# Kernel optimization log

Measured on AMD Instinct MI355X. Metric: run time of the kernel, lower is better.

Reference implementation:

```python
import jax, jax.numpy as jnp
import numpy as np

T, B, OBS, H, A = 1024, 512, 64, 128, 16


def setup_inputs() -> dict:
    key = jax.random.key(0)
    ks = jax.random.split(key, 20)
    s = lambda fan_in: 1.0 / np.sqrt(fan_in)
    return {
        "hidden": jnp.zeros((B, H), jnp.float32),
        "obs": jax.random.normal(ks[0], (T, B, OBS), jnp.float32),
        "dones": jax.random.bernoulli(ks[1], 0.05, (T, B)),
        # embedding Dense
        "W_emb": jax.random.normal(ks[2], (OBS, H), jnp.float32) * s(OBS),
        "b_emb": jnp.zeros((H,), jnp.float32),
        # GRUCell: input kernels (r|z|n) with bias, hidden kernels (r|z|n), only n-gate hidden bias
        "Wi": jax.random.normal(ks[3], (H, 3 * H), jnp.float32) * s(H),
        "bi": jnp.zeros((3 * H,), jnp.float32),
        "Wh": jax.random.normal(ks[4], (H, 3 * H), jnp.float32) * s(H),
        "bh_n": jnp.zeros((H,), jnp.float32),
        # actor head
        "Wa1": jax.random.normal(ks[5], (H, H), jnp.float32) * s(H),
        "ba1": jnp.zeros((H,), jnp.float32),
        "Wa2": jax.random.normal(ks[6], (H, A), jnp.float32) * (0.01 * s(H)),
        "ba2": jnp.zeros((A,), jnp.float32),
        # critic head
        "Wc1": jax.random.normal(ks[7], (H, H), jnp.float32) * s(H),
        "bc1": jnp.zeros((H,), jnp.float32),
        "Wc2": jax.random.normal(ks[8], (H, 1), jnp.float32) * s(H),
        "bc2": jnp.zeros((1,), jnp.float32),
    }


def reference(hidden, obs, dones, W_emb, b_emb, Wi, bi, Wh, bh_n,
              Wa1, ba1, Wa2, ba2, Wc1, bc1, Wc2, bc2):
    # embedding: Dense + relu, applied to all timesteps at once  [T,B,H]
    emb = jax.nn.relu(jnp.einsum("tbo,oh->tbh", obs, W_emb) + b_emb)
    # precompute input-side gate projections for all steps  [T,B,3H]
    xi = jnp.einsum("tbh,hg->tbg", emb, Wi) + bi

    def step(h, xs):
        xi_t, done_t = xs
        h = jnp.where(done_t[:, None], 0.0, h)  # reset carry on done
        hh = h @ Wh  # [B,3H]
        xr, xz, xn = jnp.split(xi_t, 3, axis=-1)
        hr, hz, hn = jnp.split(hh, 3, axis=-1)
        r = jax.nn.sigmoid(xr + hr)
        z = jax.nn.sigmoid(xz + hz)
        n = jnp.tanh(xn + r * (hn + bh_n))
        h_new = (1.0 - z) * n + z * h
        return h_new, h_new

    hidden, y = jax.lax.scan(step, hidden, (xi, dones))  # y: [T,B,H]

    # actor head -> categorical logits [T,B,A]
    a1 = jax.nn.relu(jnp.einsum("tbh,hk->tbk", y, Wa1) + ba1)
    logits = jnp.einsum("tbh,ha->tba", a1, Wa2) + ba2
    # critic head -> value [T,B]
    c1 = jax.nn.relu(jnp.einsum("tbh,hk->tbk", y, Wc1) + bc1)
    v = jnp.squeeze(jnp.einsum("tbh,hk->tbk", c1, Wc2) + bc2, axis=-1)
    return (hidden, logits, v)
```

## Files before the change

### kernel.cpp

```cpp
#include <hip/hip_runtime.h>

#define T_DIM 1024
#define B_DIM 512
#define OBS_DIM 64
#define H_DIM 128
#define G3 384
#define A_DIM 16
#define CT 256
#define NCHUNK 4

typedef __bf16 bf16;
typedef __attribute__((ext_vector_type(4))) __bf16 bf16x4;
typedef __attribute__((ext_vector_type(8))) __bf16 bf16x8;
typedef __attribute__((ext_vector_type(4))) float f32x4;

#define MFMA(a, b, c) __builtin_amdgcn_mfma_f32_16x16x32_bf16((a), (b), (c), 0, 0, 0)

__device__ __forceinline__ float sigm(float x) { return 1.0f / (1.0f + __expf(-x)); }
__device__ __forceinline__ float tanh_f(float x) { return 1.0f - 2.0f / (__expf(2.0f * x) + 1.0f); }

__global__ __launch_bounds__(256) void prep_k(
    const float* __restrict__ hidden, const int* __restrict__ dones,
    const float* __restrict__ W_emb, const float* __restrict__ Wi,
    const float* __restrict__ Wh, const float* __restrict__ Wa1,
    const float* __restrict__ Wa2, const float* __restrict__ Wc1,
    const float* __restrict__ Wc2,
    bf16* __restrict__ wembT, bf16* __restrict__ wiT, bf16* __restrict__ whT,
    bf16* __restrict__ wa1T, bf16* __restrict__ wa2T, bf16* __restrict__ wc1T,
    bf16* __restrict__ wc2T, float* __restrict__ h_state) {
  int i = blockIdx.x * 256 + threadIdx.x;
  if (i < 8192) { int n = i / OBS_DIM, k = i % OBS_DIM; wembT[i] = (bf16)W_emb[k * H_DIM + n]; return; }
  i -= 8192;
  if (i < 49152) { int g = i / H_DIM, k = i % H_DIM; wiT[i] = (bf16)Wi[k * G3 + g]; return; }
  i -= 49152;
  if (i < 49152) { int g = i / H_DIM, k = i % H_DIM; whT[i] = (bf16)Wh[k * G3 + g]; return; }
  i -= 49152;
  if (i < 16384) { int n = i / H_DIM, k = i % H_DIM; wa1T[i] = (bf16)Wa1[k * H_DIM + n]; return; }
  i -= 16384;
  if (i < 2048) { int a = i / H_DIM, k = i % H_DIM; wa2T[i] = (bf16)Wa2[k * A_DIM + a]; return; }
  i -= 2048;
  if (i < 16384) { int n = i / H_DIM, k = i % H_DIM; wc1T[i] = (bf16)Wc1[k * H_DIM + n]; return; }
  i -= 16384;
  if (i < 2048) { int r = i / H_DIM, k = i % H_DIM; wc2T[i] = (r == 0) ? (bf16)Wc2[k] : (bf16)0.0f; return; }
  i -= 2048;
  if (i < 65536) { int b = i / H_DIM; h_state[i] = dones[b] ? 0.0f : hidden[i]; return; }
}


__device__ __forceinline__ void phase1_body(
    char* smem, int tile_base, int ntiles, const float* __restrict__ obs,
    const float* __restrict__ b_emb, const float* __restrict__ bi,
    const bf16* __restrict__ wembT, const bf16* __restrict__ wiT,
    bf16* __restrict__ xi, int row_base) {
  bf16 (*obs_lds)[72]  = (bf16(*)[72])smem;
  bf16 (*emb_lds)[136] = (bf16(*)[136])(smem + 2304);
  bf16 (*strip)[392]   = (bf16(*)[392])(smem + 6656);
  int tid = threadIdx.x, wave = tid >> 6, lane = tid & 63;
  int nl = lane & 15, q = lane >> 4;

  bf16x8 we[2][2], wi_f[6][4];
  float bev[2], biv[6];
#pragma unroll
  for (int e = 0; e < 2; ++e) {
    int nt = wave * 2 + e;
#pragma unroll
    for (int kb = 0; kb < 2; ++kb)
      we[e][kb] = *(const bf16x8*)(wembT + (nt * 16 + nl) * OBS_DIM + kb * 32 + q * 8);
    bev[e] = b_emb[nt * 16 + nl];
  }
#pragma unroll
  for (int j = 0; j < 6; ++j) {
    int nt = wave * 6 + j;
#pragma unroll
    for (int kb = 0; kb < 4; ++kb)
      wi_f[j][kb] = *(const bf16x8*)(wiT + (nt * 16 + nl) * H_DIM + kb * 32 + q * 8);
    biv[j] = bi[nt * 16 + nl];
  }

  int srow = tid >> 4, scol = (tid & 15) * 4;
  for (int rt = 0; rt < ntiles; ++rt) {
    int r0 = (tile_base + rt) * 16;
    {
      const float* src = obs + ((long)row_base + r0 + srow) * OBS_DIM + scol;
      float4 vv = *(const float4*)src;
      bf16x4 b; b[0] = (bf16)vv.x; b[1] = (bf16)vv.y; b[2] = (bf16)vv.z; b[3] = (bf16)vv.w;
      *(bf16x4*)&obs_lds[srow][scol] = b;
    }
    __syncthreads();
    bf16x8 ao[2];
#pragma unroll
    for (int kb = 0; kb < 2; ++kb) ao[kb] = *(const bf16x8*)&obs_lds[nl][kb * 32 + q * 8];
#pragma unroll
    for (int e = 0; e < 2; ++e) {
      f32x4 c = {0.f, 0.f, 0.f, 0.f};
      c = MFMA(ao[0], we[e][0], c);
      c = MFMA(ao[1], we[e][1], c);
#pragma unroll
      for (int r = 0; r < 4; ++r) {
        float v = c[r] + bev[e];
        emb_lds[q * 4 + r][(wave * 2 + e) * 16 + nl] = (bf16)(v > 0.f ? v : 0.f);
      }
    }
    __syncthreads();
    bf16x8 ae[4];
#pragma unroll
    for (int kb = 0; kb < 4; ++kb) ae[kb] = *(const bf16x8*)&emb_lds[nl][kb * 32 + q * 8];
#pragma unroll
    for (int j = 0; j < 6; ++j) {
      int nt = wave * 6 + j;
      f32x4 c = {0.f, 0.f, 0.f, 0.f};
#pragma unroll
      for (int kb = 0; kb < 4; ++kb) c = MFMA(ae[kb], wi_f[j][kb], c);
      int gate = nt >> 3, dloc = (nt & 7) * 16 + nl;
      int pos = (gate < 2) ? (2 * dloc + gate) : (256 + dloc);
#pragma unroll
      for (int r = 0; r < 4; ++r) strip[q * 4 + r][pos] = (bf16)(c[r] + biv[j]);
    }
    __syncthreads();
    bf16* dst = xi + (long)r0 * G3;
#pragma unroll
    for (int it = 0; it < 3; ++it) {
      int e0 = (it * 256 + tid) * 8;
      int row = e0 / G3, col = e0 % G3;
      *(int4*)(dst + e0) = *(const int4*)&strip[row][col];
    }
    __syncthreads();
  }
}

__device__ __forceinline__ void scan_body(
    char* smem, int bid, const bf16* __restrict__ xi,
    const int* __restrict__ dones, const float* __restrict__ bh_n,
    const bf16* __restrict__ whT, float* __restrict__ h_state,
    bf16* __restrict__ y, float* __restrict__ hidden_out, int chunk) {
  bf16 (*hb)[2][136]       = (bf16(*)[2][136])smem;
  bf16 (*xibuf)[8][2][400] = (bf16(*)[8][2][400])(smem + 1088);
  int  (*dn)[2]            = (int(*)[2])(smem + 26688);

  __builtin_amdgcn_s_setprio(1);

  int tid = threadIdx.x;
  int wave = tid >> 6, lane = tid & 63;
  int nl = lane & 15, q = lane >> 4;
  int b0 = bid * 2;
  int ch = q & 1;
  int hsel = q >> 1;
  int dim = wave * 16 + (hsel << 6) + nl;
  int hrow = nl & 1;

  for (int i = tid; i <= CT; i += 256) {
    int t = chunk * CT + i;
    dn[i][0] = (t < T_DIM) ? dones[t * B_DIM + b0] : 0;
    dn[i][1] = (t < T_DIM) ? dones[t * B_DIM + b0 + 1] : 0;
  }
  int c0 = tid, c1 = 256 + tid, c2 = 512 + tid;
  int t0 = c0 / 96, p0 = c0 % 96, sc0 = p0 / 48, o0 = (p0 % 48) * 8;
  int t1 = c1 / 96, p1 = c1 % 96, sc1 = p1 / 48, o1 = (p1 % 48) * 8;
  int t2 = c2 / 96, p2 = c2 % 96, sc2 = p2 / 48, o2 = (p2 % 48) * 8;
  const long PSTR = (long)8 * B_DIM * G3;
  const bf16* pfs0 = xi + ((long)(8 + t0) * B_DIM + b0 + sc0) * G3 + o0;
  const bf16* pfs1 = xi + ((long)(8 + t1) * B_DIM + b0 + sc1) * G3 + o1;
  const bf16* pfs2 = xi + ((long)(8 + t2) * B_DIM + b0 + sc2) * G3 + o2;
  *(int4*)&xibuf[0][t0][sc0][o0] = *(const int4*)(xi + ((long)t0 * B_DIM + b0 + sc0) * G3 + o0);
  *(int4*)&xibuf[0][t1][sc1][o1] = *(const int4*)(xi + ((long)t1 * B_DIM + b0 + sc1) * G3 + o1);
  *(int4*)&xibuf[0][t2][sc2][o2] = *(const int4*)(xi + ((long)t2 * B_DIM + b0 + sc2) * G3 + o2);

  float hprev = h_state[(b0 + ch) * H_DIM + dim];
  hb[0][ch][dim] = (bf16)hprev;

  bf16x8 wf[6][4];
#pragma unroll
  for (int g = 0; g < 3; ++g)
#pragma unroll
    for (int hI = 0; hI < 2; ++hI)
#pragma unroll
      for (int kb = 0; kb < 4; ++kb)
        wf[g * 2 + hI][kb] =
            *(const bf16x8*)(whT + ((g * 8 + wave + 4 * hI) * 16 + nl) * H_DIM + kb * 32 + q * 8);
  float bhn = bh_n[dim];
  bf16* yp = y + (long)(b0 + ch) * H_DIM + dim;
  __syncthreads();

  int4 pfr0, pfr1, pfr2;

#define BAR()                                                                  \
  do {                                                                         \
    asm volatile("s_waitcnt lgkmcnt(0)" ::: "memory");                         \
    __builtin_amdgcn_sched_barrier(0);                                         \
    __builtin_amdgcn_s_barrier();                                              \
    __builtin_amdgcn_sched_barrier(0);                                         \
  } while (0)

#define MSTEP(HA, KB)                                                          \
  do {                                                                         \
    c0_ = MFMA(HA, wf[0][KB], c0_); c1_ = MFMA(HA, wf[1][KB], c1_);            \
    c2_ = MFMA(HA, wf[2][KB], c2_); c3_ = MFMA(HA, wf[3][KB], c3_);            \
    c4_ = MFMA(HA, wf[4][KB], c4_); c5_ = MFMA(HA, wf[5][KB], c5_);            \
  } while (0)

#define GSTEP(CUR, TS, TB, PF)                                                 \
  do {                                                                         \
    const int p_ = (TS) & 1;                                                   \
    bf16x8 ha0 = *(const bf16x8*)&hb[p_][hrow][0 * 32 + q * 8];                \
    bf16x8 ha1 = *(const bf16x8*)&hb[p_][hrow][1 * 32 + q * 8];                \
    bf16x8 ha2 = *(const bf16x8*)&hb[p_][hrow][2 * 32 + q * 8];                \
    bf16x8 ha3 = *(const bf16x8*)&hb[p_][hrow][3 * 32 + q * 8];                \
    const bf16* xrow_ = &xibuf[CUR][TS][ch][0];                                \
    unsigned urz_ = *(const unsigned*)(xrow_ + 2 * dim);                       \
    float xnv_ = (float)xrow_[256 + dim];                                      \
    int dnv_ = dn[(TB) + (TS) + 1][ch];                                        \
    if ((TS) == 0 && (PF)) {                                                   \
      pfr0 = *(const int4*)pfs0; pfs0 += PSTR;                                 \
      pfr1 = *(const int4*)pfs1; pfs1 += PSTR;                                 \
      pfr2 = *(const int4*)pfs2; pfs2 += PSTR;                                 \
    }                                                                          \
    f32x4 c0_ = {0.f, 0.f, 0.f, 0.f}, c1_ = {0.f, 0.f, 0.f, 0.f};             \
    f32x4 c2_ = {0.f, 0.f, 0.f, 0.f}, c3_ = {0.f, 0.f, 0.f, 0.f};             \
    f32x4 c4_ = {0.f, 0.f, 0.f, 0.f}, c5_ = {0.f, 0.f, 0.f, 0.f};             \
    MSTEP(ha0, 0); MSTEP(ha1, 1); MSTEP(ha2, 2); MSTEP(ha3, 3);                \
    if ((TS) == 7 && (PF)) {                                                   \
      *(int4*)&xibuf[(CUR) ^ 1][t0][sc0][o0] = pfr0;                           \
      *(int4*)&xibuf[(CUR) ^ 1][t1][sc1][o1] = pfr1;                           \
      *(int4*)&xibuf[(CUR) ^ 1][t2][sc2][o2] = pfr2;                           \
    }                                                                          \
    float hr_ = hsel ? (ch ? c1_[1] : c1_[0]) : (ch ? c0_[1] : c0_[0]);        \
    float hz_ = hsel ? (ch ? c3_[1] : c3_[0]) : (ch ? c2_[1] : c2_[0]);        \
    float hn_ = hsel ? (ch ? c5_[1] : c5_[0]) : (ch ? c4_[1] : c4_[0]);        \
    union { unsigned u; float f; } cvr_, cvz_;                                 \
    cvr_.u = urz_ << 16; cvz_.u = urz_ & 0xffff0000u;                          \
    float r_ = sigm(cvr_.f + hr_);                                             \
    float z_ = sigm(cvz_.f + hz_);                                             \
    float n_ = tanh_f(xnv_ + r_ * (hn_ + bhn));                                \
    float hnew_ = (1.0f - z_) * n_ + z_ * hprev;                               \
    float heff_ = dnv_ ? 0.0f : hnew_;                                         \
    *yp = (bf16)hnew_; yp += B_DIM * H_DIM;                                    \
    hb[p_ ^ 1][ch][dim] = (bf16)heff_;                                         \
    hprev = heff_;                                                             \
    BAR();                                                                     \
  } while (0)

  for (int tb = 0; tb < CT; tb += 16) {
    GSTEP(0, 0, tb, 1); GSTEP(0, 1, tb, 1); GSTEP(0, 2, tb, 1); GSTEP(0, 3, tb, 1);
    GSTEP(0, 4, tb, 1); GSTEP(0, 5, tb, 1); GSTEP(0, 6, tb, 1); GSTEP(0, 7, tb, 1);
    const int pfB = (tb + 16 < CT) ? 1 : 0;
    GSTEP(1, 0, tb + 8, pfB); GSTEP(1, 1, tb + 8, pfB); GSTEP(1, 2, tb + 8, pfB);
    GSTEP(1, 3, tb + 8, pfB); GSTEP(1, 4, tb + 8, pfB); GSTEP(1, 5, tb + 8, pfB);
    GSTEP(1, 6, tb + 8, pfB); GSTEP(1, 7, tb + 8, pfB);
  }
#undef GSTEP
#undef MSTEP
#undef BAR
  __builtin_amdgcn_s_setprio(0);

  h_state[(b0 + ch) * H_DIM + dim] = hprev;
  if (chunk == NCHUNK - 1) hidden_out[(b0 + ch) * H_DIM + dim] = hprev;
}

__device__ __forceinline__ void heads_body(
    char* smem, int tile_base, int ntiles, const bf16* __restrict__ y,
    const float* __restrict__ ba1, const float* __restrict__ ba2,
    const float* __restrict__ bc1, const float* __restrict__ bc2,
    const bf16* __restrict__ wa1T, const bf16* __restrict__ wa2T,
    const bf16* __restrict__ wc1T, const bf16* __restrict__ wc2T,
    float* __restrict__ logits, float* __restrict__ v, int t_base) {
  bf16  (*y_lds)[136] = (bf16(*)[136])smem;
  bf16  (*a1s)[136]   = (bf16(*)[136])(smem + 4352);
  bf16  (*c1s)[136]   = (bf16(*)[136])(smem + 8704);
  float (*s_o)[16]    = (float(*)[16])(smem + 13056);
  float (*s_v)        = (float*)(smem + 14080);
  int tid = threadIdx.x, wave = tid >> 6, lane = tid & 63;
  int nl = lane & 15, q = lane >> 4;

  bf16x8 wa1f[2][4], wc1f[2][4], wa2f[4], wc2f[4];
  float ba1v[2], bc1v[2];
#pragma unroll
  for (int e = 0; e < 2; ++e) {
    int nt = wave * 2 + e;
#pragma unroll
    for (int kb = 0; kb < 4; ++kb) {
      wa1f[e][kb] = *(const bf16x8*)(wa1T + (nt * 16 + nl) * H_DIM + kb * 32 + q * 8);
      wc1f[e][kb] = *(const bf16x8*)(wc1T + (nt * 16 + nl) * H_DIM + kb * 32 + q * 8);
    }
    ba1v[e] = ba1[nt * 16 + nl];
    bc1v[e] = bc1[nt * 16 + nl];
  }
#pragma unroll
  for (int kb = 0; kb < 4; ++kb) {
    wa2f[kb] = *(const bf16x8*)(wa2T + nl * H_DIM + kb * 32 + q * 8);
    wc2f[kb] = *(const bf16x8*)(wc2T + nl * H_DIM + kb * 32 + q * 8);
  }
  float ba2v = ba2[nl], bc2v = bc2[0];

  int srow = tid >> 4, scol = (tid & 15) * 8;
  for (int rt = 0; rt < ntiles; ++rt) {
    int r0 = (tile_base + rt) * 16;
    long gr0 = (long)t_base * B_DIM + r0;
    *(int4*)&y_lds[srow][scol] = *(const int4*)(y + (long)(r0 + srow) * H_DIM + scol);
    __syncthreads();
    bf16x8 ya[4];
#pragma unroll
    for (int kb = 0; kb < 4; ++kb) ya[kb] = *(const bf16x8*)&y_lds[nl][kb * 32 + q * 8];
#pragma unroll
    for (int e = 0; e < 2; ++e) {
      f32x4 ca = {0.f, 0.f, 0.f, 0.f}, cc = {0.f, 0.f, 0.f, 0.f};
#pragma unroll
      for (int kb = 0; kb < 4; ++kb) {
        ca = MFMA(ya[kb], wa1f[e][kb], ca);
        cc = MFMA(ya[kb], wc1f[e][kb], cc);
      }
      int colb = (wave * 2 + e) * 16 + nl;
#pragma unroll
      for (int r = 0; r < 4; ++r) {
        float va = ca[r] + ba1v[e];
        float vc = cc[r] + bc1v[e];
        a1s[q * 4 + r][colb] = (bf16)(va > 0.f ? va : 0.f);
        c1s[q * 4 + r][colb] = (bf16)(vc > 0.f ? vc : 0.f);
      }
    }
    __syncthreads();
    if (wave == 0) {
      bf16x8 a1f[4];
#pragma unroll
      for (int kb = 0; kb < 4; ++kb) a1f[kb] = *(const bf16x8*)&a1s[nl][kb * 32 + q * 8];
      f32x4 c = {0.f, 0.f, 0.f, 0.f};
#pragma unroll
      for (int kb = 0; kb < 4; ++kb) c = MFMA(a1f[kb], wa2f[kb], c);
#pragma unroll
      for (int r = 0; r < 4; ++r) s_o[q * 4 + r][nl] = c[r] + ba2v;
    } else if (wave == 1) {
      bf16x8 c1f[4];
#pragma unroll
      for (int kb = 0; kb < 4; ++kb) c1f[kb] = *(const bf16x8*)&c1s[nl][kb * 32 + q * 8];
      f32x4 c = {0.f, 0.f, 0.f, 0.f};
#pragma unroll
      for (int kb = 0; kb < 4; ++kb) c = MFMA(c1f[kb], wc2f[kb], c);
      if (nl == 0) {
#pragma unroll
        for (int r = 0; r < 4; ++r) s_v[q * 4 + r] = c[r] + bc2v;
      }
    }
    __syncthreads();
    if (tid < 64) {
      *(int4*)(logits + gr0 * A_DIM + tid * 4) = *(const int4*)&s_o[tid >> 2][(tid & 3) * 4];
    } else if (tid < 80) {
      v[gr0 + (tid - 64)] = s_v[tid - 64];
    }
    __syncthreads();
  }
}

__global__ __launch_bounds__(256, 2) void fused_k(
    const float* __restrict__ obs, const float* __restrict__ b_emb,
    const float* __restrict__ bi, const bf16* __restrict__ wembT,
    const bf16* __restrict__ wiT, bf16* __restrict__ xi0, bf16* __restrict__ xi1,
    const int* __restrict__ dones, const float* __restrict__ bh_n,
    const bf16* __restrict__ whT, float* __restrict__ h_state,
    bf16* __restrict__ y0, bf16* __restrict__ y1, float* __restrict__ hidden_out,
    const float* __restrict__ ba1, const float* __restrict__ ba2,
    const float* __restrict__ bc1, const float* __restrict__ bc2,
    const bf16* __restrict__ wa1T, const bf16* __restrict__ wa2T,
    const bf16* __restrict__ wc1T, const bf16* __restrict__ wc2T,
    float* __restrict__ logits, float* __restrict__ v, int cs) {
  __shared__ __align__(16) char smem[50176];
  int bid = blockIdx.x;
  if (cs == -1) {
    phase1_body(smem, bid * 16, 16, obs, b_emb, bi, wembT, wiT, xi0, 0);
    return;
  }
  if (cs == NCHUNK) {
    heads_body(smem, bid * 16, 16, ((NCHUNK - 1) & 1) ? y1 : y0, ba1, ba2, bc1,
               bc2, wa1T, wa2T, wc1T, wc2T, logits, v, (NCHUNK - 1) * CT);
    return;
  }
  if (bid < 256) {
    scan_body(smem, bid, (cs & 1) ? xi1 : xi0, dones, bh_n, whT, h_state,
              (cs & 1) ? y1 : y0, hidden_out, cs);
    return;
  }
  {
    int wb = bid - 256;
    int cp = cs + 1;
    if (cp < NCHUNK)
      phase1_body(smem, wb * 32, 32, obs, b_emb, bi, wembT, wiT,
                  (cp & 1) ? xi1 : xi0, cp * CT * B_DIM);
    int ch2 = cs - 1;
    if (ch2 >= 0)
      heads_body(smem, wb * 32, 32, (ch2 & 1) ? y1 : y0, ba1, ba2, bc1, bc2,
                 wa1T, wa2T, wc1T, wc2T, logits, v, ch2 * CT);
  }
}

extern "C" void kernel_launch(void* const* d_in, const int* in_sizes, int n_in,
                              void* d_out, int out_size, void* d_ws, size_t ws_size,
                              hipStream_t stream) {
  const float* hidden = (const float*)d_in[0];
  const float* obs    = (const float*)d_in[1];
  const int*   dones  = (const int*)d_in[2];
  const float* W_emb  = (const float*)d_in[3];
  const float* b_emb  = (const float*)d_in[4];
  const float* Wi     = (const float*)d_in[5];
  const float* bi     = (const float*)d_in[6];
  const float* Wh     = (const float*)d_in[7];
  const float* bh_n   = (const float*)d_in[8];
  const float* Wa1    = (const float*)d_in[9];
  const float* ba1    = (const float*)d_in[10];
  const float* Wa2    = (const float*)d_in[11];
  const float* ba2    = (const float*)d_in[12];
  const float* Wc1    = (const float*)d_in[13];
  const float* bc1    = (const float*)d_in[14];
  const float* Wc2    = (const float*)d_in[15];
  const float* bc2    = (const float*)d_in[16];

  float* out_hidden = (float*)d_out;
  float* out_logits = out_hidden + B_DIM * H_DIM;
  float* out_v      = out_logits + (long)T_DIM * B_DIM * A_DIM;

  char* ws = (char*)d_ws;
  bf16*  wembT   = (bf16*)(ws + 0);
  bf16*  wiT     = (bf16*)(ws + 16384);
  bf16*  whT     = (bf16*)(ws + 114688);
  bf16*  wa1T    = (bf16*)(ws + 212992);
  bf16*  wa2T    = (bf16*)(ws + 245760);
  bf16*  wc1T    = (bf16*)(ws + 249856);
  bf16*  wc2T    = (bf16*)(ws + 282624);
  float* h_state = (float*)(ws + 286720);
  bf16*  xi0     = (bf16*)(ws + 548864);
  bf16*  xi1     = (bf16*)(ws + 101212160);
  bf16*  y0      = (bf16*)(ws + 201875456);
  bf16*  y1      = (bf16*)(ws + 235429888);

  prep_k<<<816, 256, 0, stream>>>(hidden, dones, W_emb, Wi, Wh, Wa1, Wa2, Wc1, Wc2,
                                  wembT, wiT, whT, wa1T, wa2T, wc1T, wc2T, h_state);
  for (int cs = -1; cs <= NCHUNK; ++cs) {
    fused_k<<<512, 256, 0, stream>>>(obs, b_emb, bi, wembT, wiT, xi0, xi1,
                                     dones, bh_n, whT, h_state, y0, y1, out_hidden,
                                     ba1, ba2, bc1, bc2, wa1T, wa2T, wc1T, wc2T,
                                     out_logits, out_v, cs);
  }
  (void)in_sizes; (void)n_in; (void)out_size; (void)ws_size;
}
```

Baseline: 748.1 us.

## Process four batch rows per scan block and halve grid to one block per CU

Each scan block now handles 4 batch rows instead of 2, using all four lanes groups of the MFMA output and computing two hidden dims per lane. The grid shrinks to 256 blocks (128 scan + 128 producer/heads) with launch bounds of one block per CU and a smaller LDS footprint, and prefetch blocks become 4 timesteps. This halves the number of weight-register copies and uses the MFMA rows more fully, but doubles the serial elementwise work per lane per step and reduces overall parallelism for the non-scan phases.

New measurement: 977.1 us. 1.31x slower.

```diff
diff --git a/kernel.cpp b/kernel.cpp
--- a/kernel.cpp
+++ b/kernel.cpp
@@ -18,6 +18,11 @@
 
 __device__ __forceinline__ float sigm(float x) { return 1.0f / (1.0f + __expf(-x)); }
 __device__ __forceinline__ float tanh_f(float x) { return 1.0f - 2.0f / (__expf(2.0f * x) + 1.0f); }
+__device__ __forceinline__ float sel4(f32x4 v, int qa, int qb) {
+  float lo = qa ? v[1] : v[0];
+  float hi = qa ? v[3] : v[2];
+  return qb ? hi : lo;
+}
 
 __global__ __launch_bounds__(256) void prep_k(
     const float* __restrict__ hidden, const int* __restrict__ dones,
@@ -133,40 +138,41 @@
     const int* __restrict__ dones, const float* __restrict__ bh_n,
     const bf16* __restrict__ whT, float* __restrict__ h_state,
     bf16* __restrict__ y, float* __restrict__ hidden_out, int chunk) {
-  bf16 (*hb)[2][136]       = (bf16(*)[2][136])smem;
-  bf16 (*xibuf)[8][2][400] = (bf16(*)[8][2][400])(smem + 1088);
-  int  (*dn)[2]            = (int(*)[2])(smem + 26688);
+  bf16 (*hb)[4][136]       = (bf16(*)[4][136])smem;
+  bf16 (*xibuf)[4][4][400] = (bf16(*)[4][4][400])(smem + 2176);
+  int  (*dn)[4]            = (int(*)[4])(smem + 27776);
 
   __builtin_amdgcn_s_setprio(1);
 
   int tid = threadIdx.x;
   int wave = tid >> 6, lane = tid & 63;
   int nl = lane & 15, q = lane >> 4;
-  int b0 = bid * 2;
-  int ch = q & 1;
-  int hsel = q >> 1;
-  int dim = wave * 16 + (hsel << 6) + nl;
-  int hrow = nl & 1;
+  int b0 = bid * 4;
+  int d0 = wave * 16 + nl, d1 = d0 + 64;
+  int hrow = nl & 3;
+  int qa = q & 1, qb = q >> 1;
 
   for (int i = tid; i <= CT; i += 256) {
     int t = chunk * CT + i;
-    dn[i][0] = (t < T_DIM) ? dones[t * B_DIM + b0] : 0;
-    dn[i][1] = (t < T_DIM) ? dones[t * B_DIM + b0 + 1] : 0;
+    if (t < T_DIM) *(int4*)&dn[i][0] = *(const int4*)&dones[t * B_DIM + b0];
+    else { dn[i][0] = 0; dn[i][1] = 0; dn[i][2] = 0; dn[i][3] = 0; }
   }
   int c0 = tid, c1 = 256 + tid, c2 = 512 + tid;
-  int t0 = c0 / 96, p0 = c0 % 96, sc0 = p0 / 48, o0 = (p0 % 48) * 8;
-  int t1 = c1 / 96, p1 = c1 % 96, sc1 = p1 / 48, o1 = (p1 % 48) * 8;
-  int t2 = c2 / 96, p2 = c2 % 96, sc2 = p2 / 48, o2 = (p2 % 48) * 8;
-  const long PSTR = (long)8 * B_DIM * G3;
-  const bf16* pfs0 = xi + ((long)(8 + t0) * B_DIM + b0 + sc0) * G3 + o0;
-  const bf16* pfs1 = xi + ((long)(8 + t1) * B_DIM + b0 + sc1) * G3 + o1;
-  const bf16* pfs2 = xi + ((long)(8 + t2) * B_DIM + b0 + sc2) * G3 + o2;
+  int t0 = c0 / 192, r0_ = c0 % 192, sc0 = r0_ / 48, o0 = (r0_ % 48) * 8;
+  int t1 = c1 / 192, r1_ = c1 % 192, sc1 = r1_ / 48, o1 = (r1_ % 48) * 8;
+  int t2 = c2 / 192, r2_ = c2 % 192, sc2 = r2_ / 48, o2 = (r2_ % 48) * 8;
+  const long PSTR = (long)4 * B_DIM * G3;
+  const bf16* pfs0 = xi + ((long)(4 + t0) * B_DIM + b0 + sc0) * G3 + o0;
+  const bf16* pfs1 = xi + ((long)(4 + t1) * B_DIM + b0 + sc1) * G3 + o1;
+  const bf16* pfs2 = xi + ((long)(4 + t2) * B_DIM + b0 + sc2) * G3 + o2;
   *(int4*)&xibuf[0][t0][sc0][o0] = *(const int4*)(xi + ((long)t0 * B_DIM + b0 + sc0) * G3 + o0);
   *(int4*)&xibuf[0][t1][sc1][o1] = *(const int4*)(xi + ((long)t1 * B_DIM + b0 + sc1) * G3 + o1);
   *(int4*)&xibuf[0][t2][sc2][o2] = *(const int4*)(xi + ((long)t2 * B_DIM + b0 + sc2) * G3 + o2);
 
-  float hprev = h_state[(b0 + ch) * H_DIM + dim];
-  hb[0][ch][dim] = (bf16)hprev;
+  float hprev0 = h_state[(b0 + q) * H_DIM + d0];
+  float hprev1 = h_state[(b0 + q) * H_DIM + d1];
+  hb[0][q][d0] = (bf16)hprev0;
+  hb[0][q][d1] = (bf16)hprev1;
 
   bf16x8 wf[6][4];
 #pragma unroll
@@ -177,8 +183,10 @@
       for (int kb = 0; kb < 4; ++kb)
         wf[g * 2 + hI][kb] =
             *(const bf16x8*)(whT + ((g * 8 + wave + 4 * hI) * 16 + nl) * H_DIM + kb * 32 + q * 8);
-  float bhn = bh_n[dim];
-  bf16* yp = y + (long)(b0 + ch) * H_DIM + dim;
+  float bhn0 = bh_n[d0], bhn1 = bh_n[d1];
+  bf16* yp0 = y + (long)(b0 + q) * H_DIM + d0;
+  bf16* yp1 = y + (long)(b0 + q) * H_DIM + d1;
+  const f32x4 zero = {0.f, 0.f, 0.f, 0.f};
   __syncthreads();
 
   int4 pfr0, pfr1, pfr2;
@@ -205,55 +213,65 @@
     bf16x8 ha1 = *(const bf16x8*)&hb[p_][hrow][1 * 32 + q * 8];                \
     bf16x8 ha2 = *(const bf16x8*)&hb[p_][hrow][2 * 32 + q * 8];                \
     bf16x8 ha3 = *(const bf16x8*)&hb[p_][hrow][3 * 32 + q * 8];                \
-    const bf16* xrow_ = &xibuf[CUR][TS][ch][0];                                \
-    unsigned urz_ = *(const unsigned*)(xrow_ + 2 * dim);                       \
-    float xnv_ = (float)xrow_[256 + dim];                                      \
-    int dnv_ = dn[(TB) + (TS) + 1][ch];                                        \
+    const bf16* xrow_ = &xibuf[CUR][TS][q][0];                                 \
+    unsigned urz0_ = *(const unsigned*)(xrow_ + 2 * d0);                       \
+    unsigned urz1_ = *(const unsigned*)(xrow_ + 2 * d1);                       \
+    float xn0_ = (float)xrow_[256 + d0];                                       \
+    float xn1_ = (float)xrow_[256 + d1];                                       \
+    int dnv_ = dn[(TB) + (TS) + 1][q];                                         \
     if ((TS) == 0 && (PF)) {                                                   \
       pfr0 = *(const int4*)pfs0; pfs0 += PSTR;                                 \
       pfr1 = *(const int4*)pfs1; pfs1 += PSTR;                                 \
       pfr2 = *(const int4*)pfs2; pfs2 += PSTR;                                 \
     }                                                                          \
-    f32x4 c0_ = {0.f, 0.f, 0.f, 0.f}, c1_ = {0.f, 0.f, 0.f, 0.f};             \
-    f32x4 c2_ = {0.f, 0.f, 0.f, 0.f}, c3_ = {0.f, 0.f, 0.f, 0.f};             \
-    f32x4 c4_ = {0.f, 0.f, 0.f, 0.f}, c5_ = {0.f, 0.f, 0.f, 0.f};             \
-    MSTEP(ha0, 0); MSTEP(ha1, 1); MSTEP(ha2, 2); MSTEP(ha3, 3);                \
-    if ((TS) == 7 && (PF)) {                                                   \
+    f32x4 c0_ = MFMA(ha0, wf[0][0], zero), c1_ = MFMA(ha0, wf[1][0], zero);    \
+    f32x4 c2_ = MFMA(ha0, wf[2][0], zero), c3_ = MFMA(ha0, wf[3][0], zero);    \
+    f32x4 c4_ = MFMA(ha0, wf[4][0], zero), c5_ = MFMA(ha0, wf[5][0], zero);    \
+    MSTEP(ha1, 1); MSTEP(ha2, 2); MSTEP(ha3, 3);                               \
+    if ((TS) == 3 && (PF)) {                                                   \
       *(int4*)&xibuf[(CUR) ^ 1][t0][sc0][o0] = pfr0;                           \
       *(int4*)&xibuf[(CUR) ^ 1][t1][sc1][o1] = pfr1;                           \
       *(int4*)&xibuf[(CUR) ^ 1][t2][sc2][o2] = pfr2;                           \
     }                                                                          \
-    float hr_ = hsel ? (ch ? c1_[1] : c1_[0]) : (ch ? c0_[1] : c0_[0]);        \
-    float hz_ = hsel ? (ch ? c3_[1] : c3_[0]) : (ch ? c2_[1] : c2_[0]);        \
-    float hn_ = hsel ? (ch ? c5_[1] : c5_[0]) : (ch ? c4_[1] : c4_[0]);        \
-    union { unsigned u; float f; } cvr_, cvz_;                                 \
-    cvr_.u = urz_ << 16; cvz_.u = urz_ & 0xffff0000u;                          \
-    float r_ = sigm(cvr_.f + hr_);                                             \
-    float z_ = sigm(cvz_.f + hz_);                                             \
-    float n_ = tanh_f(xnv_ + r_ * (hn_ + bhn));                                \
-    float hnew_ = (1.0f - z_) * n_ + z_ * hprev;                               \
-    float heff_ = dnv_ ? 0.0f : hnew_;                                         \
-    *yp = (bf16)hnew_; yp += B_DIM * H_DIM;                                    \
-    hb[p_ ^ 1][ch][dim] = (bf16)heff_;                                         \
-    hprev = heff_;                                                             \
+    float hr0_ = sel4(c0_, qa, qb), hr1_ = sel4(c1_, qa, qb);                  \
+    float hz0_ = sel4(c2_, qa, qb), hz1_ = sel4(c3_, qa, qb);                  \
+    float hn0_ = sel4(c4_, qa, qb), hn1_ = sel4(c5_, qa, qb);                  \
+    union { unsigned u; float f; } a0u_, b0u_, a1u_, b1u_;                     \
+    a0u_.u = urz0_ << 16; b0u_.u = urz0_ & 0xffff0000u;                        \
+    a1u_.u = urz1_ << 16; b1u_.u = urz1_ & 0xffff0000u;                        \
+    float r0g_ = sigm(a0u_.f + hr0_), r1g_ = sigm(a1u_.f + hr1_);              \
+    float z0g_ = sigm(b0u_.f + hz0_), z1g_ = sigm(b1u_.f + hz1_);              \
+    float n0g_ = tanh_f(xn0_ + r0g_ * (hn0_ + bhn0));                          \
+    float n1g_ = tanh_f(xn1_ + r1g_ * (hn1_ + bhn1));                          \
+    float hnew0_ = (1.0f - z0g_) * n0g_ + z0g_ * hprev0;                       \
+    float hnew1_ = (1.0f - z1g_) * n1g_ + z1g_ * hprev1;                       \
+    float heff0_ = dnv_ ? 0.0f : hnew0_;                                       \
+    float heff1_ = dnv_ ? 0.0f : hnew1_;                                       \
+    *yp0 = (bf16)hnew0_; yp0 += B_DIM * H_DIM;                                 \
+    *yp1 = (bf16)hnew1_; yp1 += B_DIM * H_DIM;                                 \
+    hb[p_ ^ 1][q][d0] = (bf16)heff0_;                                          \
+    hb[p_ ^ 1][q][d1] = (bf16)heff1_;                                          \
+    hprev0 = heff0_; hprev1 = heff1_;                                          \
     BAR();                                                                     \
   } while (0)
 
-  for (int tb = 0; tb < CT; tb += 16) {
+  for (int tb = 0; tb < CT; tb += 8) {
     GSTEP(0, 0, tb, 1); GSTEP(0, 1, tb, 1); GSTEP(0, 2, tb, 1); GSTEP(0, 3, tb, 1);
-    GSTEP(0, 4, tb, 1); GSTEP(0, 5, tb, 1); GSTEP(0, 6, tb, 1); GSTEP(0, 7, tb, 1);
-    const int pfB = (tb + 16 < CT) ? 1 : 0;
-    GSTEP(1, 0, tb + 8, pfB); GSTEP(1, 1, tb + 8, pfB); GSTEP(1, 2, tb + 8, pfB);
-    GSTEP(1, 3, tb + 8, pfB); GSTEP(1, 4, tb + 8, pfB); GSTEP(1, 5, tb + 8, pfB);
-    GSTEP(1, 6, tb + 8, pfB); GSTEP(1, 7, tb + 8, pfB);
+    const int pfB = (tb + 8 < CT) ? 1 : 0;
+    GSTEP(1, 0, tb + 4, pfB); GSTEP(1, 1, tb + 4, pfB);
+    GSTEP(1, 2, tb + 4, pfB); GSTEP(1, 3, tb + 4, pfB);
   }
 #undef GSTEP
 #undef MSTEP
 #undef BAR
   __builtin_amdgcn_s_setprio(0);
 
-  h_state[(b0 + ch) * H_DIM + dim] = hprev;
-  if (chunk == NCHUNK - 1) hidden_out[(b0 + ch) * H_DIM + dim] = hprev;
+  h_state[(b0 + q) * H_DIM + d0] = hprev0;
+  h_state[(b0 + q) * H_DIM + d1] = hprev1;
+  if (chunk == NCHUNK - 1) {
+    hidden_out[(b0 + q) * H_DIM + d0] = hprev0;
+    hidden_out[(b0 + q) * H_DIM + d1] = hprev1;
+  }
 }
 
 __device__ __forceinline__ void heads_body(
@@ -349,7 +367,7 @@
   }
 }
 
-__global__ __launch_bounds__(256, 2) void fused_k(
+__global__ __launch_bounds__(256, 1) void fused_k(
     const float* __restrict__ obs, const float* __restrict__ b_emb,
     const float* __restrict__ bi, const bf16* __restrict__ wembT,
     const bf16* __restrict__ wiT, bf16* __restrict__ xi0, bf16* __restrict__ xi1,
@@ -361,32 +379,32 @@
     const bf16* __restrict__ wa1T, const bf16* __restrict__ wa2T,
     const bf16* __restrict__ wc1T, const bf16* __restrict__ wc2T,
     float* __restrict__ logits, float* __restrict__ v, int cs) {
-  __shared__ __align__(16) char smem[50176];
+  __shared__ __align__(16) char smem[32768];
   int bid = blockIdx.x;
   if (cs == -1) {
-    phase1_body(smem, bid * 16, 16, obs, b_emb, bi, wembT, wiT, xi0, 0);
+    phase1_body(smem, bid * 32, 32, obs, b_emb, bi, wembT, wiT, xi0, 0);
     return;
   }
   if (cs == NCHUNK) {
-    heads_body(smem, bid * 16, 16, ((NCHUNK - 1) & 1) ? y1 : y0, ba1, ba2, bc1,
+    heads_body(smem, bid * 32, 32, ((NCHUNK - 1) & 1) ? y1 : y0, ba1, ba2, bc1,
                bc2, wa1T, wa2T, wc1T, wc2T, logits, v, (NCHUNK - 1) * CT);
     return;
   }
-  if (bid < 256) {
+  if (bid < 128) {
     scan_body(smem, bid, (cs & 1) ? xi1 : xi0, dones, bh_n, whT, h_state,
               (cs & 1) ? y1 : y0, hidden_out, cs);
     return;
   }
   {
-    int wb = bid - 256;
+    int wb = bid - 128;
     int cp = cs + 1;
     if (cp < NCHUNK)
-      phase1_body(smem, wb * 32, 32, obs, b_emb, bi, wembT, wiT,
+      phase1_body(smem, wb * 64, 64, obs, b_emb, bi, wembT, wiT,
                   (cp & 1) ? xi1 : xi0, cp * CT * B_DIM);
-    int ch2 = cs - 1;
-    if (ch2 >= 0)
-      heads_body(smem, wb * 32, 32, (ch2 & 1) ? y1 : y0, ba1, ba2, bc1, bc2,
-                 wa1T, wa2T, wc1T, wc2T, logits, v, ch2 * CT);
+    int c2 = cs - 1;
+    if (c2 >= 0)
+      heads_body(smem, wb * 64, 64, (c2 & 1) ? y1 : y0, ba1, ba2, bc1, bc2,
+                 wa1T, wa2T, wc1T, wc2T, logits, v, c2 * CT);
   }
 }
 
@@ -432,7 +450,7 @@
   prep_k<<<816, 256, 0, stream>>>(hidden, dones, W_emb, Wi, Wh, Wa1, Wa2, Wc1, Wc2,
                                   wembT, wiT, whT, wa1T, wa2T, wc1T, wc2T, h_state);
   for (int cs = -1; cs <= NCHUNK; ++cs) {
-    fused_k<<<512, 256, 0, stream>>>(obs, b_emb, bi, wembT, wiT, xi0, xi1,
+    fused_k<<<256, 256, 0, stream>>>(obs, b_emb, bi, wembT, wiT, xi0, xi1,
                                      dones, bh_n, whT, h_state, y0, y1, out_hidden,
                                      ba1, ba2, bc1, bc2, wa1T, wa2T, wc1T, wc2T,
                                      out_logits, out_v, cs);
```
